# Optimization experiments

Hardware: AMD Instinct MI355X
Metric: run time of the kernel (lower is better)

## Reference

```python
import jax, jax.numpy as jnp
import numpy as np

N, H, W, K = 8, 512, 512, 4
F_FACES, V_VERTS, D = 200000, 100000, 3


def setup_inputs() -> dict:
    key = jax.random.key(0)
    k1, k2, k3, k4 = jax.random.split(key, 4)
    pix_to_face = jax.random.randint(k1, (N, H, W, K), 0, F_FACES, dtype=jnp.int64 if jax.config.jax_enable_x64 else jnp.int32)
    bg = jax.random.uniform(k2, (N, H, W, K)) < 0.2
    pix_to_face = jnp.where(bg, -1, pix_to_face)
    bary_raw = jax.random.uniform(k2, (N, H, W, K, 3))
    bary_coords = bary_raw / jnp.sum(bary_raw, axis=-1, keepdims=True)  # convex weights
    faces = jax.random.randint(k3, (F_FACES, 3), 0, V_VERTS)
    verts_colors = jax.random.uniform(k4, (V_VERTS, D))
    return {
        "pix_to_face": pix_to_face,
        "bary_coords": bary_coords,
        "faces": faces,
        "verts_colors": verts_colors,
    }


def reference(pix_to_face, bary_coords, faces, verts_colors):
    # face_colors: [F, 3, D] -- per-face vertex colors
    face_colors = verts_colors[faces]
    mask = pix_to_face >= 0  # [N,H,W,K]
    idx = jnp.where(mask, pix_to_face, 0)
    # gather per-pixel per-sample face colors: [N,H,W,K,3,D]
    gathered = face_colors[idx]
    # barycentric weighted sum over the 3 face vertices -> [N,H,W,K,D]
    pixel_colors = jnp.einsum("nhwkv,nhwkvd->nhwkd", bary_coords, gathered)
    pixel_colors = jnp.where(mask[..., None], pixel_colors, 0.0)
    # return top (closest) face sample K=0
    return pixel_colors[..., 0, :]
```

## Files before the change

kernel.cpp:

```cpp
#include <hip/hip_runtime.h>


#define NPIX (8 * 512 * 512)

__global__ __launch_bounds__(256) void unlit_shader_kernel(
    const int* __restrict__ p2f,
    const float* __restrict__ bary,
    const int* __restrict__ faces,
    const float* __restrict__ vc,
    float* __restrict__ out)
{
    const int p = blockIdx.x * 256 + threadIdx.x;
    if (p >= NPIX) return;

    const int f = p2f[(size_t)p * 4];

    const float4 b = *reinterpret_cast<const float4*>(bary + (size_t)p * 12);

    float r0 = 0.0f, r1 = 0.0f, r2 = 0.0f;
    if (f >= 0) {
        const int* fv = faces + (size_t)f * 3;
        const int v0 = fv[0];
        const int v1 = fv[1];
        const int v2 = fv[2];
        const float* c0 = vc + (size_t)v0 * 3;
        const float* c1 = vc + (size_t)v1 * 3;
        const float* c2 = vc + (size_t)v2 * 3;
        r0 = b.x * c0[0] + b.y * c1[0] + b.z * c2[0];
        r1 = b.x * c0[1] + b.y * c1[1] + b.z * c2[1];
        r2 = b.x * c0[2] + b.y * c1[2] + b.z * c2[2];
    }

    float* o = out + (size_t)p * 3;
    o[0] = r0;
    o[1] = r1;
    o[2] = r2;
}

extern "C" void kernel_launch(void* const* d_in, const int* in_sizes, int n_in,
                              void* d_out, int out_size, void* d_ws, size_t ws_size,
                              hipStream_t stream) {
    const int*   p2f   = (const int*)d_in[0];
    const float* bary  = (const float*)d_in[1];
    const int*   faces = (const int*)d_in[2];
    const float* vc    = (const float*)d_in[3];
    float*       out   = (float*)d_out;

    const int blocks = NPIX / 256;
    unlit_shader_kernel<<<blocks, 256, 0, stream>>>(p2f, bary, faces, vc, out);
}
```

Measured before the change: 207.1 us.

## Precompute per-face vertex colors into padded float4 table before shading

Adds a pre-pass that gathers each face's three vertex colors into a contiguous float4-padded table in the workspace. The shading kernel then does a single indirection per pixel with vector loads, instead of a dependent faces-then-vertices gather chain. This costs an extra kernel launch and about 9.6MB of writes per call. If the workspace is too small, it falls back to the direct kernel.

```diff
diff --git a/kernel.cpp b/kernel.cpp
--- a/kernel.cpp
+++ b/kernel.cpp
@@ -2,8 +2,57 @@
 
 
 #define NPIX (8 * 512 * 512)
+#define F_FACES 200000
 
-__global__ __launch_bounds__(256) void unlit_shader_kernel(
+__global__ __launch_bounds__(256) void repack_face_colors_kernel(
+    const int* __restrict__ faces,
+    const float* __restrict__ vc,
+    float4* __restrict__ fc)
+{
+    const int f = blockIdx.x * 256 + threadIdx.x;
+    if (f >= F_FACES) return;
+    const int v0 = faces[(size_t)f * 3 + 0];
+    const int v1 = faces[(size_t)f * 3 + 1];
+    const int v2 = faces[(size_t)f * 3 + 2];
+    const float* c0 = vc + (size_t)v0 * 3;
+    const float* c1 = vc + (size_t)v1 * 3;
+    const float* c2 = vc + (size_t)v2 * 3;
+    float4* o = fc + (size_t)f * 3;
+    o[0] = make_float4(c0[0], c0[1], c0[2], 0.0f);
+    o[1] = make_float4(c1[0], c1[1], c1[2], 0.0f);
+    o[2] = make_float4(c2[0], c2[1], c2[2], 0.0f);
+}
+
+__global__ __launch_bounds__(256) void shade_kernel(
+    const int* __restrict__ p2f,
+    const float* __restrict__ bary,
+    const float4* __restrict__ fc,
+    float* __restrict__ out)
+{
+    const int p = blockIdx.x * 256 + threadIdx.x;
+    if (p >= NPIX) return;
+
+    const int f = p2f[(size_t)p * 4];
+    const float4 b = *reinterpret_cast<const float4*>(bary + (size_t)p * 12);
+
+    float r0 = 0.0f, r1 = 0.0f, r2 = 0.0f;
+    if (f >= 0) {
+        const float4* c = fc + (size_t)f * 3;
+        const float4 c0 = c[0];
+        const float4 c1 = c[1];
+        const float4 c2 = c[2];
+        r0 = b.x * c0.x + b.y * c1.x + b.z * c2.x;
+        r1 = b.x * c0.y + b.y * c1.y + b.z * c2.y;
+        r2 = b.x * c0.z + b.y * c1.z + b.z * c2.z;
+    }
+
+    float* o = out + (size_t)p * 3;
+    o[0] = r0;
+    o[1] = r1;
+    o[2] = r2;
+}
+
+__global__ __launch_bounds__(256) void shade_direct_kernel(
     const int* __restrict__ p2f,
     const float* __restrict__ bary,
     const int* __restrict__ faces,
@@ -12,25 +61,18 @@
 {
     const int p = blockIdx.x * 256 + threadIdx.x;
     if (p >= NPIX) return;
-
     const int f = p2f[(size_t)p * 4];
-
     const float4 b = *reinterpret_cast<const float4*>(bary + (size_t)p * 12);
-
     float r0 = 0.0f, r1 = 0.0f, r2 = 0.0f;
     if (f >= 0) {
         const int* fv = faces + (size_t)f * 3;
-        const int v0 = fv[0];
-        const int v1 = fv[1];
-        const int v2 = fv[2];
-        const float* c0 = vc + (size_t)v0 * 3;
-        const float* c1 = vc + (size_t)v1 * 3;
-        const float* c2 = vc + (size_t)v2 * 3;
+        const float* c0 = vc + (size_t)fv[0] * 3;
+        const float* c1 = vc + (size_t)fv[1] * 3;
+        const float* c2 = vc + (size_t)fv[2] * 3;
         r0 = b.x * c0[0] + b.y * c1[0] + b.z * c2[0];
         r1 = b.x * c0[1] + b.y * c1[1] + b.z * c2[1];
         r2 = b.x * c0[2] + b.y * c1[2] + b.z * c2[2];
     }
-
     float* o = out + (size_t)p * 3;
     o[0] = r0;
     o[1] = r1;
@@ -46,6 +88,13 @@
     const float* vc    = (const float*)d_in[3];
     float*       out   = (float*)d_out;
 
-    const int blocks = NPIX / 256;
-    unlit_shader_kernel<<<blocks, 256, 0, stream>>>(p2f, bary, faces, vc, out);
+    const size_t fc_bytes = (size_t)F_FACES * 3 * sizeof(float4);
+
+    if (ws_size >= fc_bytes) {
+        float4* fc = (float4*)d_ws;
+        repack_face_colors_kernel<<<(F_FACES + 255) / 256, 256, 0, stream>>>(faces, vc, fc);
+        shade_kernel<<<NPIX / 256, 256, 0, stream>>>(p2f, bary, fc, out);
+    } else {
+        shade_direct_kernel<<<NPIX / 256, 256, 0, stream>>>(p2f, bary, faces, vc, out);
+    }
 }
```

New measurement: 193.7 us. 1.07x faster.
